# Kernel tuning notes

Hardware: AMD Instinct MI355X
Metric: run time of the kernel (lower is better)

Reference implementation:

```python
import jax, jax.numpy as jnp
import numpy as np

T = 20
DT = 0.001
TAU = 0.02
V_TH = 0.5
V_RESET = 0.0


def setup_inputs() -> dict:
    key = jax.random.key(0)
    ks = jax.random.split(key, 5)
    batch, embed_dim, expert_dim, num_experts, hidden_dim = 256, 1024, 64, 16, 1024
    return {
        "query_embedding": jax.random.normal(ks[0], (batch, embed_dim), dtype=jnp.float32),
        "gate_bias": jax.random.normal(ks[1], (num_experts,), dtype=jnp.float32),
        "temperature": jnp.ones((1,), dtype=jnp.float32),
        "W_in": jax.random.normal(ks[2], (embed_dim, expert_dim), dtype=jnp.float32) * 0.03,
        "experts": jax.random.normal(ks[3], (num_experts, expert_dim, hidden_dim), dtype=jnp.float32) * 0.1,
        "gate_kernel": jax.random.normal(ks[4], (expert_dim, num_experts), dtype=jnp.float32) * 0.1,
    }


def reference(query_embedding, gate_bias, temperature, W_in, experts, gate_kernel):
    dtype = query_embedding.dtype
    x = (query_embedding @ W_in).astype(dtype)  # [B, D]

    # Poisson encoding: Bernoulli spikes with rate sigmoid(x), fixed module key.
    rates = jax.nn.sigmoid(x)
    _, bern_key = jax.random.split(jax.random.key(0))
    input_spikes = jax.random.bernoulli(bern_key, rates, shape=(T,) + rates.shape).astype(dtype)  # [T, B, D]

    # Softmax MoE gate (computed in fp32 as in original).
    gate_logits = x @ gate_kernel + gate_bias[None, :].astype(dtype)  # [B, E]
    gate_probs = jax.nn.softmax(
        gate_logits.astype(jnp.float32) / temperature.astype(jnp.float32), axis=-1
    ).astype(dtype)

    E, _, H = experts.shape
    B = x.shape[0]
    leak = DT / TAU

    def time_step(v, s_t):
        # v: [E, B, H]; s_t: [B, D]
        current = jnp.einsum('bd,edh->ebh', s_t, experts)
        new_v = v + (current - v) * leak
        spike = (new_v >= V_TH).astype(dtype)
        new_v = new_v * (1.0 - spike) + V_RESET * spike
        return new_v, spike

    v0 = jnp.zeros((E, B, H), dtype=dtype)
    _, spikes_all = jax.lax.scan(time_step, v0, input_spikes)  # [T, E, B, H]

    avg_spikes = jnp.mean(spikes_all, axis=0)  # [E, B, H]
    # Gate-weighted combine over experts -> [B, H]
    return jnp.einsum('ebh,be->bh', avg_spikes, gate_probs)
```

## Files before the change

kernel.cpp:

```cpp
#include <hip/hip_runtime.h>

typedef unsigned int u32;
typedef unsigned short u16;
typedef unsigned char u8;
typedef __attribute__((ext_vector_type(8))) short bf16x8;
typedef __attribute__((ext_vector_type(4))) float f32x4;

#define JAX_PARTITIONABLE 1
#define FLAG_DELTA 5e-4f
#define FLAG_CAP 262144u

__host__ __device__ static inline void tf2x32(u32 k0, u32 k1, u32 x0, u32 x1,
                                              u32* o0, u32* o1)
{
  const u32 ks2 = k0 ^ k1 ^ 0x1BD11BDAu;
#define TF_R(v, r) (((v) << (r)) | ((v) >> (32 - (r))))
#define TF_RND(r) do { x0 += x1; x1 = TF_R(x1, r); x1 ^= x0; } while (0);
  x0 += k0; x1 += k1;
  TF_RND(13) TF_RND(15) TF_RND(26) TF_RND(6)
  x0 += k1;  x1 += ks2 + 1u;
  TF_RND(17) TF_RND(29) TF_RND(16) TF_RND(24)
  x0 += ks2; x1 += k0 + 2u;
  TF_RND(13) TF_RND(15) TF_RND(26) TF_RND(6)
  x0 += k0;  x1 += k1 + 3u;
  TF_RND(17) TF_RND(29) TF_RND(16) TF_RND(24)
  x0 += k1;  x1 += ks2 + 4u;
  TF_RND(13) TF_RND(15) TF_RND(26) TF_RND(6)
  x0 += ks2; x1 += k0 + 5u;
  *o0 = x0; *o1 = x1;
#undef TF_RND
#undef TF_R
}

__device__ static inline u16 f2bf(float f) {
  u32 u = __float_as_uint(f);
  return (u16)((u + 0x7FFFu + ((u >> 16) & 1u)) >> 16);
}
__device__ static inline float bf2f(u16 b) {
  return __uint_as_float(((u32)b) << 16);
}

__global__ __launch_bounds__(256) void k_gate(
    const float* __restrict__ q, const float* __restrict__ win,
    const float* __restrict__ gbias, const float* __restrict__ temp,
    const float* __restrict__ gk, float* __restrict__ rates,
    float* __restrict__ gateo, u32* __restrict__ fcnt)
{
  const int tid = threadIdx.x;
  if (blockIdx.x == 0 && tid == 0) fcnt[0] = 0;
  __shared__ float qs[4][1024];
  const int b4 = blockIdx.x * 4;
#pragma unroll
  for (int r = 0; r < 4; ++r) {
    const float4 qv = *(const float4*)(q + (size_t)(b4 + r) * 1024 + tid * 4);
    *(float4*)(&qs[r][tid * 4]) = qv;
  }
  __syncthreads();

  const int w = tid >> 6, j = tid & 63;
  const int b = b4 + w;
  const float* __restrict__ wc = win + j;
  float bufA[64], bufB[64];
#pragma unroll
  for (int i = 0; i < 64; ++i) bufA[i] = wc[i * 64];
  float c = 0.f;
#pragma unroll
  for (int ch = 0; ch < 8; ++ch) {
#pragma unroll
    for (int i = 0; i < 64; ++i)
      bufB[i] = wc[((2 * ch + 1) * 64 + i) * 64];
#pragma unroll
    for (int i = 0; i < 64; ++i)
      c = __builtin_fmaf(qs[w][2 * ch * 64 + i], bufA[i], c);
    if (ch < 7) {
#pragma unroll
      for (int i = 0; i < 64; ++i)
        bufA[i] = wc[((2 * ch + 2) * 64 + i) * 64];
    }
#pragma unroll
    for (int i = 0; i < 64; ++i)
      c = __builtin_fmaf(qs[w][(2 * ch + 1) * 64 + i], bufB[i], c);
  }
  const float x = c;
  float r;
  if (x >= 0.f) r = __fdiv_rn(1.f, __fadd_rn(1.f, expf(-x)));
  else { const float ex = expf(x); r = __fdiv_rn(ex, __fadd_rn(1.f, ex)); }
  rates[b * 64 + j] = r;

  const int jj = j & 15;
  float l = 0.f;
  for (int dd = 0; dd < 64; ++dd) {
    const float xv = __shfl(x, dd, 64);
    l = __builtin_fmaf(xv, gk[dd * 16 + jj], l);
  }
  l = __fadd_rn(l, gbias[jj]);
  l = __fdiv_rn(l, temp[0]);
  float m = l;
  for (int off = 1; off < 16; off <<= 1) m = fmaxf(m, __shfl_xor(m, off, 16));
  const float p = expf(__fsub_rn(l, m));
  float s = p;
  for (int off = 1; off < 16; off <<= 1) s += __shfl_xor(s, off, 16);
  if (j < 16) gateo[b * 16 + j] = __fdiv_rn(p, s);
}

__global__ __launch_bounds__(256) void k_prep(
    const float* __restrict__ ex, u16* __restrict__ wsp, float* __restrict__ ext,
    const float* __restrict__ rates, u16* __restrict__ spk, u32 bk0, u32 bk1)
{
  if (blockIdx.x < 256) {
    const int e = blockIdx.x >> 4, hb = blockIdx.x & 15;
    const int tl = threadIdx.x & 63, tg = threadIdx.x >> 6;
    __shared__ float tile[64][65];
#pragma unroll
    for (int r = 0; r < 16; ++r) {
      const int d = r * 4 + tg;
      tile[d][tl] = ex[((size_t)e * 64 + d) * 1024 + hb * 64 + tl];
    }
    __syncthreads();
#pragma unroll
    for (int r = 0; r < 16; ++r) {
      const int hl = r * 4 + tg;
      const float wraw = tile[tl][hl];
      const float wv = wraw * 0.05f;
      const u16 hi = f2bf(wv);
      const u16 lo = f2bf(wv - bf2f(hi));
      const size_t o = ((size_t)e * 1024 + hb * 64 + hl) * 64 + tl;
      wsp[o] = hi;
      wsp[o + 1048576] = lo;
      ext[o] = wraw;
    }
  } else {
    const u32 g = (blockIdx.x - 256) * 256u + threadIdx.x;
#if JAX_PARTITIONABLE
    u32 o0, o1;
    tf2x32(bk0, bk1, 0u, g, &o0, &o1);
    const u32 bits = o0 ^ o1;
    const float r = rates[g & 16383u];
    const float u = __uint_as_float((bits >> 9) | 0x3f800000u) - 1.0f;
    spk[g] = (u < r) ? (u16)0x3F80 : (u16)0;
#else
    u32 o0, o1;
    tf2x32(bk0, bk1, g, g + 163840u, &o0, &o1);
    const float r = rates[g & 16383u];
    const float ua = __uint_as_float((o0 >> 9) | 0x3f800000u) - 1.0f;
    const float ub = __uint_as_float((o1 >> 9) | 0x3f800000u) - 1.0f;
    spk[g] = (ua < r) ? (u16)0x3F80 : (u16)0;
    spk[g + 163840u] = (ub < r) ? (u16)0x3F80 : (u16)0;
#endif
  }
}

__global__ __launch_bounds__(256) void k_lif(
    const u16* __restrict__ spk, const u16* __restrict__ wsp,
    u8* __restrict__ cnt, u32* __restrict__ fcnt, u32* __restrict__ flist)
{
  const int hblk = blockIdx.x, bblk = blockIdx.y, e = blockIdx.z;
  const int tid = threadIdx.x;
  const int w = tid >> 6, lane = tid & 63;
  const int wb = w & 1, wh = w >> 1;
  const int lr = lane & 15, lg = lane >> 4;
  const int b0 = bblk * 32 + wb * 16;
  const int h0 = hblk * 64 + wh * 32;

#define FRAG(NT, KC, S) (*(const bf16x8*)(wsp + \
    ((size_t)((S) * 16 + e) * 1024 + h0 + (NT) * 16 + lr) * 64 + (KC) * 32 + lg * 8))
  bf16x8 bh00 = FRAG(0, 0, 0), bh01 = FRAG(0, 1, 0);
  bf16x8 bh10 = FRAG(1, 0, 0), bh11 = FRAG(1, 1, 0);
  bf16x8 bl00 = FRAG(0, 0, 1), bl01 = FRAG(0, 1, 1);
  bf16x8 bl10 = FRAG(1, 0, 1), bl11 = FRAG(1, 1, 1);
#undef FRAG
  asm volatile("" : "+v"(bh00), "+v"(bh01), "+v"(bh10), "+v"(bh11));
  asm volatile("" : "+v"(bl00), "+v"(bl01), "+v"(bl10), "+v"(bl11));

  f32x4 v0 = (f32x4){0.f, 0.f, 0.f, 0.f};
  f32x4 v1 = (f32x4){0.f, 0.f, 0.f, 0.f};
  int cn[2][4];
#pragma unroll
  for (int nt = 0; nt < 2; ++nt)
#pragma unroll
    for (int i = 0; i < 4; ++i) cn[nt][i] = 0;
  u32 fl = 0;

  const u16* abase = spk + (size_t)(b0 + lr) * 64 + lg * 8;
  bf16x8 a0 = *(const bf16x8*)(abase);
  bf16x8 a1 = *(const bf16x8*)(abase + 32);

#define PROC(VAL, CREF, BIT) {                                  \
    const float tt = (VAL) - 0.5f;                              \
    if (__builtin_fabsf(tt) < FLAG_DELTA) fl |= (1u << (BIT));  \
    const bool sp = (tt >= 0.f);                                \
    (CREF) += sp;                                               \
    (VAL) = sp ? 0.f : (VAL); }

  for (int t = 0; t < 20; ++t) {
    const int tn = (t < 19) ? t + 1 : 19;
    const bf16x8 n0 = *(const bf16x8*)(abase + (size_t)tn * 16384);
    const bf16x8 n1 = *(const bf16x8*)(abase + (size_t)tn * 16384 + 32);
    {
      f32x4 accA = v0 * 0.95f;
      accA = __builtin_amdgcn_mfma_f32_16x16x32_bf16(a0, bh00, accA, 0, 0, 0);
      accA = __builtin_amdgcn_mfma_f32_16x16x32_bf16(a1, bh01, accA, 0, 0, 0);
      f32x4 accB = (f32x4){0.f, 0.f, 0.f, 0.f};
      accB = __builtin_amdgcn_mfma_f32_16x16x32_bf16(a0, bl00, accB, 0, 0, 0);
      accB = __builtin_amdgcn_mfma_f32_16x16x32_bf16(a1, bl01, accB, 0, 0, 0);
      f32x4 nv = accA + accB;
      PROC(nv.x, cn[0][0], 0)
      PROC(nv.y, cn[0][1], 1)
      PROC(nv.z, cn[0][2], 2)
      PROC(nv.w, cn[0][3], 3)
      v0 = nv;
    }
    {
      f32x4 accA = v1 * 0.95f;
      accA = __builtin_amdgcn_mfma_f32_16x16x32_bf16(a0, bh10, accA, 0, 0, 0);
      accA = __builtin_amdgcn_mfma_f32_16x16x32_bf16(a1, bh11, accA, 0, 0, 0);
      f32x4 accB = (f32x4){0.f, 0.f, 0.f, 0.f};
      accB = __builtin_amdgcn_mfma_f32_16x16x32_bf16(a0, bl10, accB, 0, 0, 0);
      accB = __builtin_amdgcn_mfma_f32_16x16x32_bf16(a1, bl11, accB, 0, 0, 0);
      f32x4 nv = accA + accB;
      PROC(nv.x, cn[1][0], 4)
      PROC(nv.y, cn[1][1], 5)
      PROC(nv.z, cn[1][2], 6)
      PROC(nv.w, cn[1][3], 7)
      v1 = nv;
    }
    a0 = n0; a1 = n1;
  }
#undef PROC

#pragma unroll
  for (int nt = 0; nt < 2; ++nt) {
    const int h = h0 + nt * 16 + lr;
#pragma unroll
    for (int i = 0; i < 4; ++i) {
      const int b = b0 + lg * 4 + i;
      cnt[((size_t)e * 256 + b) * 1024 + h] = (u8)cn[nt][i];
    }
  }

  const u32 myc = (u32)__builtin_popcount((int)fl);
  u32 pre = myc;
#pragma unroll
  for (int off = 1; off < 64; off <<= 1) {
    const u32 xx = __shfl_up(pre, off, 64);
    if (lane >= off) pre += xx;
  }
  const u32 tot = __shfl(pre, 63, 64);
  if (tot) {
    u32 base = 0;
    if (lane == 63) base = atomicAdd(fcnt, tot);
    base = __shfl(base, 63, 64);
    u32 slot = base + pre - myc;
    if (fl) {
#pragma unroll
      for (int nt = 0; nt < 2; ++nt)
#pragma unroll
        for (int i = 0; i < 4; ++i)
          if ((fl >> (nt * 4 + i)) & 1u) {
            if (slot < FLAG_CAP)
              flist[slot] = ((u32)e << 18) | ((u32)(b0 + lg * 4 + i) << 10) |
                            (u32)(h0 + nt * 16 + lr);
            slot++;
          }
    }
  }
}

__global__ __launch_bounds__(256) void k_fix(
    const u16* __restrict__ spk, const float* __restrict__ ext,
    const u32* __restrict__ fcnt, const u32* __restrict__ flist,
    u8* __restrict__ cnt)
{
  u32 n = fcnt[0];
  if (n > FLAG_CAP) n = FLAG_CAP;
  for (u32 i = blockIdx.x * 256u + threadIdx.x; i < n; i += 65536u) {
    const u32 p = flist[i];
    const int h = (int)(p & 1023u), b = (int)((p >> 10) & 255u), e = (int)(p >> 18);
    const float* __restrict__ wbp = ext + ((size_t)e * 1024 + h) * 64;
    float wr[64];
#pragma unroll
    for (int d4 = 0; d4 < 16; ++d4) {
      const float4 wv = *(const float4*)(wbp + d4 * 4);
      wr[d4 * 4 + 0] = wv.x; wr[d4 * 4 + 1] = wv.y;
      wr[d4 * 4 + 2] = wv.z; wr[d4 * 4 + 3] = wv.w;
    }
    float v = 0.f;
    int c = 0;
    for (int t = 0; t < 20; ++t) {
      const uint4* __restrict__ sr = (const uint4*)(spk + (size_t)(t * 256 + b) * 64);
      float cc = 0.f;
#pragma unroll
      for (int w8 = 0; w8 < 8; ++w8) {
        const uint4 sv = sr[w8];
        cc = __builtin_fmaf(__uint_as_float(sv.x << 16),         wr[w8 * 8 + 0], cc);
        cc = __builtin_fmaf(__uint_as_float(sv.x & 0xFFFF0000u), wr[w8 * 8 + 1], cc);
        cc = __builtin_fmaf(__uint_as_float(sv.y << 16),         wr[w8 * 8 + 2], cc);
        cc = __builtin_fmaf(__uint_as_float(sv.y & 0xFFFF0000u), wr[w8 * 8 + 3], cc);
        cc = __builtin_fmaf(__uint_as_float(sv.z << 16),         wr[w8 * 8 + 4], cc);
        cc = __builtin_fmaf(__uint_as_float(sv.z & 0xFFFF0000u), wr[w8 * 8 + 5], cc);
        cc = __builtin_fmaf(__uint_as_float(sv.w << 16),         wr[w8 * 8 + 6], cc);
        cc = __builtin_fmaf(__uint_as_float(sv.w & 0xFFFF0000u), wr[w8 * 8 + 7], cc);
      }
      const float nv = __fadd_rn(v, __fmul_rn(__fsub_rn(cc, v), 0.05f));
      if (nv >= 0.5f) { c++; v = 0.f; } else v = nv;
    }
    cnt[((size_t)e * 256 + b) * 1024 + h] = (u8)c;
  }
}

__global__ __launch_bounds__(256) void k_combine(
    const u8* __restrict__ cnt, const float* __restrict__ gateo,
    float* __restrict__ out)
{
  const int idx = blockIdx.x * 256 + threadIdx.x;
  const int b = idx >> 8, hq = idx & 255;
  const int h0 = hq * 4;
  float s0 = 0.f, s1 = 0.f, s2 = 0.f, s3 = 0.f;
#pragma unroll
  for (int e = 0; e < 16; ++e) {
    const uchar4 cv = *(const uchar4*)(cnt + ((size_t)e * 256 + b) * 1024 + h0);
    const float g = gateo[b * 16 + e];
    s0 = __builtin_fmaf(__fdiv_rn((float)cv.x, 20.f), g, s0);
    s1 = __builtin_fmaf(__fdiv_rn((float)cv.y, 20.f), g, s1);
    s2 = __builtin_fmaf(__fdiv_rn((float)cv.z, 20.f), g, s2);
    s3 = __builtin_fmaf(__fdiv_rn((float)cv.w, 20.f), g, s3);
  }
  float4 o;
  o.x = s0; o.y = s1; o.z = s2; o.w = s3;
  *(float4*)(out + (size_t)b * 1024 + h0) = o;
}

extern "C" void kernel_launch(void* const* d_in, const int* in_sizes, int n_in,
                              void* d_out, int out_size, void* d_ws, size_t ws_size,
                              hipStream_t stream)
{
  (void)in_sizes; (void)n_in; (void)out_size; (void)ws_size;
  const float* q     = (const float*)d_in[0];
  const float* gbias = (const float*)d_in[1];
  const float* temp  = (const float*)d_in[2];
  const float* win   = (const float*)d_in[3];
  const float* ex    = (const float*)d_in[4];
  const float* gk    = (const float*)d_in[5];
  float* out = (float*)d_out;

  char* ws = (char*)d_ws;
  u16*  spk   = (u16*)(ws + 0);
  float* rates = (float*)(ws + 655360);
  float* gateo = (float*)(ws + 720896);
  u16*  wsp   = (u16*)(ws + 737280);
  u8*   cnt   = (u8*)(ws + 4931584);
  u32*  fcnt  = (u32*)(ws + 9125888);
  u32*  flist = (u32*)(ws + 9126912);
  float* ext  = (float*)(ws + 10175488);

  u32 bk0, bk1;
#if JAX_PARTITIONABLE
  tf2x32(0u, 0u, 0u, 1u, &bk0, &bk1);
#else
  u32 a0o, a1o, b0o, b1o;
  tf2x32(0u, 0u, 0u, 2u, &a0o, &a1o);
  tf2x32(0u, 0u, 1u, 3u, &b0o, &b1o);
  bk0 = a1o; bk1 = b1o;
#endif

  k_gate<<<64, 256, 0, stream>>>(q, win, gbias, temp, gk, rates, gateo, fcnt);
#if JAX_PARTITIONABLE
  k_prep<<<256 + 1280, 256, 0, stream>>>(ex, wsp, ext, rates, spk, bk0, bk1);
#else
  k_prep<<<256 + 640, 256, 0, stream>>>(ex, wsp, ext, rates, spk, bk0, bk1);
#endif
  k_lif<<<dim3(16, 8, 16), 256, 0, stream>>>(spk, wsp, cnt, fcnt, flist);
  k_fix<<<256, 256, 0, stream>>>(spk, ext, fcnt, flist, cnt);
  k_combine<<<256, 256, 0, stream>>>(cnt, gateo, out);
}
```

Baseline: 195.7 us.

## Drop bf16 hi/lo weight split in LIF matmul and widen flag band

The expert weights are now stored as a single bf16 value instead of a hi/lo pair. This halves the MFMA work and the weight fragment registers in the LIF recurrence. To absorb the larger rounding error, the band around the threshold that sends neurons to the exact fp32 fix-up pass widens from 5e-4 to 2e-2. Each wave now covers 64 hidden columns with packed byte counters, the grid shrinks to match, and launch bounds request 4 waves. The trade-off is many more flagged entries for k_fix to recompute, and possible overflow of the flag list cap, which would hurt correctness.

Result: slower. 210.6 us (+7.7%).

```diff
diff --git a/kernel.cpp b/kernel.cpp
--- a/kernel.cpp
+++ b/kernel.cpp
@@ -7,7 +7,7 @@
 typedef __attribute__((ext_vector_type(4))) float f32x4;
 
 #define JAX_PARTITIONABLE 1
-#define FLAG_DELTA 5e-4f
+#define FLAG_DELTA 2e-2f
 #define FLAG_CAP 262144u
 
 __host__ __device__ static inline void tf2x32(u32 k0, u32 k1, u32 x0, u32 x1,
@@ -36,9 +36,6 @@
   u32 u = __float_as_uint(f);
   return (u16)((u + 0x7FFFu + ((u >> 16) & 1u)) >> 16);
 }
-__device__ static inline float bf2f(u16 b) {
-  return __uint_as_float(((u32)b) << 16);
-}
 
 __global__ __launch_bounds__(256) void k_gate(
     const float* __restrict__ q, const float* __restrict__ win,
@@ -121,12 +118,8 @@
     for (int r = 0; r < 16; ++r) {
       const int hl = r * 4 + tg;
       const float wraw = tile[tl][hl];
-      const float wv = wraw * 0.05f;
-      const u16 hi = f2bf(wv);
-      const u16 lo = f2bf(wv - bf2f(hi));
       const size_t o = ((size_t)e * 1024 + hb * 64 + hl) * 64 + tl;
-      wsp[o] = hi;
-      wsp[o + 1048576] = lo;
+      wsp[o] = f2bf(wraw * 0.05f);
       ext[o] = wraw;
     }
   } else {
@@ -150,7 +143,7 @@
   }
 }
 
-__global__ __launch_bounds__(256) void k_lif(
+__global__ __launch_bounds__(256, 4) void k_lif(
     const u16* __restrict__ spk, const u16* __restrict__ wsp,
     u8* __restrict__ cnt, u32* __restrict__ fcnt, u32* __restrict__ flist)
 {
@@ -160,81 +153,65 @@
   const int wb = w & 1, wh = w >> 1;
   const int lr = lane & 15, lg = lane >> 4;
   const int b0 = bblk * 32 + wb * 16;
-  const int h0 = hblk * 64 + wh * 32;
-
-#define FRAG(NT, KC, S) (*(const bf16x8*)(wsp + \
-    ((size_t)((S) * 16 + e) * 1024 + h0 + (NT) * 16 + lr) * 64 + (KC) * 32 + lg * 8))
-  bf16x8 bh00 = FRAG(0, 0, 0), bh01 = FRAG(0, 1, 0);
-  bf16x8 bh10 = FRAG(1, 0, 0), bh11 = FRAG(1, 1, 0);
-  bf16x8 bl00 = FRAG(0, 0, 1), bl01 = FRAG(0, 1, 1);
-  bf16x8 bl10 = FRAG(1, 0, 1), bl11 = FRAG(1, 1, 1);
+  const int h0 = hblk * 128 + wh * 64;
+
+#define FRAG(NT, KC) (*(const bf16x8*)(wsp + \
+    ((size_t)e * 1024 + h0 + (NT) * 16 + lr) * 64 + (KC) * 32 + lg * 8))
+  bf16x8 b00 = FRAG(0, 0), b01 = FRAG(0, 1);
+  bf16x8 b10 = FRAG(1, 0), b11 = FRAG(1, 1);
+  bf16x8 b20 = FRAG(2, 0), b21 = FRAG(2, 1);
+  bf16x8 b30 = FRAG(3, 0), b31 = FRAG(3, 1);
 #undef FRAG
-  asm volatile("" : "+v"(bh00), "+v"(bh01), "+v"(bh10), "+v"(bh11));
-  asm volatile("" : "+v"(bl00), "+v"(bl01), "+v"(bl10), "+v"(bl11));
+  asm volatile("" : "+v"(b00), "+v"(b01), "+v"(b10), "+v"(b11));
+  asm volatile("" : "+v"(b20), "+v"(b21), "+v"(b30), "+v"(b31));
 
   f32x4 v0 = (f32x4){0.f, 0.f, 0.f, 0.f};
-  f32x4 v1 = (f32x4){0.f, 0.f, 0.f, 0.f};
-  int cn[2][4];
-#pragma unroll
-  for (int nt = 0; nt < 2; ++nt)
-#pragma unroll
-    for (int i = 0; i < 4; ++i) cn[nt][i] = 0;
+  f32x4 v1 = v0, v2 = v0, v3 = v0;
+  u32 c0 = 0, c1 = 0, c2 = 0, c3 = 0;
   u32 fl = 0;
 
   const u16* abase = spk + (size_t)(b0 + lr) * 64 + lg * 8;
   bf16x8 a0 = *(const bf16x8*)(abase);
   bf16x8 a1 = *(const bf16x8*)(abase + 32);
 
-#define PROC(VAL, CREF, BIT) {                                  \
+#define PROC(VAL, CW, I, BIT) {                                 \
     const float tt = (VAL) - 0.5f;                              \
     if (__builtin_fabsf(tt) < FLAG_DELTA) fl |= (1u << (BIT));  \
     const bool sp = (tt >= 0.f);                                \
-    (CREF) += sp;                                               \
+    (CW) += ((u32)sp) << (8 * (I));                             \
     (VAL) = sp ? 0.f : (VAL); }
+
+#define STEP(VV, CW, BL, BH, NT) {                                          \
+    f32x4 acc = (VV) * 0.95f;                                               \
+    acc = __builtin_amdgcn_mfma_f32_16x16x32_bf16(a0, (BL), acc, 0, 0, 0);  \
+    acc = __builtin_amdgcn_mfma_f32_16x16x32_bf16(a1, (BH), acc, 0, 0, 0);  \
+    PROC(acc.x, (CW), 0, (NT) * 4 + 0)                                      \
+    PROC(acc.y, (CW), 1, (NT) * 4 + 1)                                      \
+    PROC(acc.z, (CW), 2, (NT) * 4 + 2)                                      \
+    PROC(acc.w, (CW), 3, (NT) * 4 + 3)                                      \
+    (VV) = acc; }
 
   for (int t = 0; t < 20; ++t) {
     const int tn = (t < 19) ? t + 1 : 19;
     const bf16x8 n0 = *(const bf16x8*)(abase + (size_t)tn * 16384);
     const bf16x8 n1 = *(const bf16x8*)(abase + (size_t)tn * 16384 + 32);
-    {
-      f32x4 accA = v0 * 0.95f;
-      accA = __builtin_amdgcn_mfma_f32_16x16x32_bf16(a0, bh00, accA, 0, 0, 0);
-      accA = __builtin_amdgcn_mfma_f32_16x16x32_bf16(a1, bh01, accA, 0, 0, 0);
-      f32x4 accB = (f32x4){0.f, 0.f, 0.f, 0.f};
-      accB = __builtin_amdgcn_mfma_f32_16x16x32_bf16(a0, bl00, accB, 0, 0, 0);
-      accB = __builtin_amdgcn_mfma_f32_16x16x32_bf16(a1, bl01, accB, 0, 0, 0);
-      f32x4 nv = accA + accB;
-      PROC(nv.x, cn[0][0], 0)
-      PROC(nv.y, cn[0][1], 1)
-      PROC(nv.z, cn[0][2], 2)
-      PROC(nv.w, cn[0][3], 3)
-      v0 = nv;
-    }
-    {
-      f32x4 accA = v1 * 0.95f;
-      accA = __builtin_amdgcn_mfma_f32_16x16x32_bf16(a0, bh10, accA, 0, 0, 0);
-      accA = __builtin_amdgcn_mfma_f32_16x16x32_bf16(a1, bh11, accA, 0, 0, 0);
-      f32x4 accB = (f32x4){0.f, 0.f, 0.f, 0.f};
-      accB = __builtin_amdgcn_mfma_f32_16x16x32_bf16(a0, bl10, accB, 0, 0, 0);
-      accB = __builtin_amdgcn_mfma_f32_16x16x32_bf16(a1, bl11, accB, 0, 0, 0);
-      f32x4 nv = accA + accB;
-      PROC(nv.x, cn[1][0], 4)
-      PROC(nv.y, cn[1][1], 5)
-      PROC(nv.z, cn[1][2], 6)
-      PROC(nv.w, cn[1][3], 7)
-      v1 = nv;
-    }
+    STEP(v0, c0, b00, b01, 0)
+    STEP(v1, c1, b10, b11, 1)
+    STEP(v2, c2, b20, b21, 2)
+    STEP(v3, c3, b30, b31, 3)
     a0 = n0; a1 = n1;
   }
+#undef STEP
 #undef PROC
 
-#pragma unroll
-  for (int nt = 0; nt < 2; ++nt) {
+  const u32 cw[4] = {c0, c1, c2, c3};
+#pragma unroll
+  for (int nt = 0; nt < 4; ++nt) {
     const int h = h0 + nt * 16 + lr;
 #pragma unroll
     for (int i = 0; i < 4; ++i) {
       const int b = b0 + lg * 4 + i;
-      cnt[((size_t)e * 256 + b) * 1024 + h] = (u8)cn[nt][i];
+      cnt[((size_t)e * 256 + b) * 1024 + h] = (u8)((cw[nt] >> (8 * i)) & 0xFFu);
     }
   }
 
@@ -253,7 +230,7 @@
     u32 slot = base + pre - myc;
     if (fl) {
 #pragma unroll
-      for (int nt = 0; nt < 2; ++nt)
+      for (int nt = 0; nt < 4; ++nt)
 #pragma unroll
         for (int i = 0; i < 4; ++i)
           if ((fl >> (nt * 4 + i)) & 1u) {
@@ -348,10 +325,10 @@
   float* rates = (float*)(ws + 655360);
   float* gateo = (float*)(ws + 720896);
   u16*  wsp   = (u16*)(ws + 737280);
-  u8*   cnt   = (u8*)(ws + 4931584);
-  u32*  fcnt  = (u32*)(ws + 9125888);
-  u32*  flist = (u32*)(ws + 9126912);
-  float* ext  = (float*)(ws + 10175488);
+  u8*   cnt   = (u8*)(ws + 2834432);
+  u32*  fcnt  = (u32*)(ws + 7028736);
+  u32*  flist = (u32*)(ws + 7029760);
+  float* ext  = (float*)(ws + 8078336);
 
   u32 bk0, bk1;
 #if JAX_PARTITIONABLE
@@ -369,7 +346,7 @@
 #else
   k_prep<<<256 + 640, 256, 0, stream>>>(ex, wsp, ext, rates, spk, bk0, bk1);
 #endif
-  k_lif<<<dim3(16, 8, 16), 256, 0, stream>>>(spk, wsp, cnt, fcnt, flist);
+  k_lif<<<dim3(8, 8, 16), 256, 0, stream>>>(spk, wsp, cnt, fcnt, flist);
   k_fix<<<256, 256, 0, stream>>>(spk, ext, fcnt, flist, cnt);
   k_combine<<<256, 256, 0, stream>>>(cnt, gateo, out);
 }
```
